# Kernel tuning notes

Measured on AMD Instinct MI355X. Metric: run time of the kernel, lower is better.

## Reference

```python
import jax, jax.numpy as jnp
import numpy as np
import math

D_MODEL = 1024
N_HEADS = 16
HEAD_DIM = D_MODEL // N_HEADS
SEQ = 2048
BATCH = 4
MAX_SEQ_LEN = 2048
THETA = 10000.0


def setup_inputs() -> dict:
    key = jax.random.key(0)
    ks = jax.random.split(key, 5)
    std = math.sqrt(2.0 / (D_MODEL + D_MODEL))
    x = jax.random.normal(ks[0], (BATCH, SEQ, D_MODEL), dtype=jnp.float32)
    wq = jax.random.normal(ks[1], (D_MODEL, D_MODEL), dtype=jnp.float32) * std
    wk = jax.random.normal(ks[2], (D_MODEL, D_MODEL), dtype=jnp.float32) * std
    wv = jax.random.normal(ks[3], (D_MODEL, D_MODEL), dtype=jnp.float32) * std
    wo = jax.random.normal(ks[4], (D_MODEL, D_MODEL), dtype=jnp.float32) * std
    token_positions = jnp.arange(SEQ, dtype=jnp.int32)
    return {"x": x, "token_positions": token_positions,
            "wq": wq, "wk": wk, "wv": wv, "wo": wo}


def _rope_tables(token_positions):
    # thetas_i = 1 / theta^(2i/d_k), angles[p, i] = p * thetas_i
    thetas = 1.0 / (THETA ** (2.0 * jnp.arange(HEAD_DIM // 2, dtype=jnp.float32) / HEAD_DIM))
    positions = jnp.arange(MAX_SEQ_LEN, dtype=jnp.float32)
    angles = jnp.outer(positions, thetas)  # [max_seq, d_k/2]
    cos = jnp.cos(angles)[token_positions]  # [S, d_k/2]
    sin = jnp.sin(angles)[token_positions]
    return cos, sin


def _apply_rope(x, cos, sin):
    # x: [B, H, S, D]; pairs (even, odd) form complex numbers
    shp = x.shape
    x2 = x.reshape(*shp[:-1], HEAD_DIM // 2, 2)
    xe, xo = x2[..., 0], x2[..., 1]
    re = xe * cos - xo * sin
    im = xe * sin + xo * cos
    return jnp.stack([re, im], axis=-1).reshape(shp)


def reference(x, token_positions, wq, wk, wv, wo):
    B, S, _ = x.shape
    # LinearNoBias: einsum('...j,ij->...i', x, W)
    q = jnp.einsum('bsj,ij->bsi', x, wq)
    k = jnp.einsum('bsj,ij->bsi', x, wk)
    v = jnp.einsum('bsj,ij->bsi', x, wv)
    # split heads -> [B, H, S, D]
    q = q.reshape(B, S, N_HEADS, HEAD_DIM).transpose(0, 2, 1, 3)
    k = k.reshape(B, S, N_HEADS, HEAD_DIM).transpose(0, 2, 1, 3)
    v = v.reshape(B, S, N_HEADS, HEAD_DIM).transpose(0, 2, 1, 3)
    cos, sin = _rope_tables(token_positions)
    q = _apply_rope(q, cos, sin)
    k = _apply_rope(k, cos, sin)
    scores = jnp.einsum('bhqd,bhkd->bhqk', q, k) / math.sqrt(HEAD_DIM)
    causal = jnp.tril(jnp.ones((S, S), dtype=bool))
    scores = jnp.where(causal, scores, -jnp.inf)
    probs = jax.nn.softmax(scores, axis=-1)
    out = jnp.einsum('bhqk,bhkd->bhqd', probs, v)
    out = out.transpose(0, 2, 1, 3).reshape(B, S, N_HEADS * HEAD_DIM)
    return jnp.einsum('bsj,ij->bsi', out, wo)
```

## Files before the change

### kernel.cpp

```cpp
#include <hip/hip_runtime.h>
#include <stdint.h>

#define B_SZ 4
#define S_LEN 2048
#define NH 16
#define HD 64
#define DM 1024

typedef __bf16 bf16;
typedef __bf16 bf16x4 __attribute__((ext_vector_type(4)));
typedef __bf16 bf16x8 __attribute__((ext_vector_type(8)));
typedef float f32x4 __attribute__((ext_vector_type(4)));

#define MFMA16(a, b, c) __builtin_amdgcn_mfma_f32_16x16x32_bf16(a, b, c, 0, 0, 0)

__device__ __forceinline__ void gl2lds16(const void* g, void* l) {
  __builtin_amdgcn_global_load_lds(
      (__attribute__((address_space(1))) const void*)g,
      (__attribute__((address_space(3))) void*)l, 16, 0, 0);
}

__device__ __forceinline__ void bar_lgkm() {
  asm volatile("s_waitcnt lgkmcnt(0)\n\ts_barrier" ::: "memory");
}

__device__ __forceinline__ bf16x8 ldcvt(const float* p) {
  f32x4 u0 = *(const f32x4*)p;
  f32x4 u1 = *(const f32x4*)(p + 4);
  bf16x8 v;
#pragma unroll
  for (int j = 0; j < 4; j++) {
    v[j] = (bf16)u0[j];
    v[4 + j] = (bf16)u1[j];
  }
  return v;
}

__global__ void cvt_kernel(const float* __restrict__ x,
                           const float* __restrict__ wq,
                           const float* __restrict__ wk,
                           const float* __restrict__ wv,
                           const float* __restrict__ wo,
                           bf16* __restrict__ Xb, bf16* __restrict__ Wb,
                           long xN) {
  const long e = ((long)blockIdx.x * 256 + threadIdx.x) * 8;
  const float* src;
  bf16* dst;
  long off;
  if (e < xN) {
    src = x; dst = Xb; off = e;
  } else {
    const long w = e - xN;
    const int wi = (int)(w >> 20);
    src = (wi == 0) ? wq : (wi == 1) ? wk : (wi == 2) ? wv : wo;
    dst = Wb + ((size_t)wi << 20);
    off = w & ((1L << 20) - 1);
  }
  *(bf16x8*)(dst + off) = ldcvt(src + off);
}

__device__ __forceinline__ void gemm_core_bb(const bf16* __restrict__ Ag,
                                             const bf16* __restrict__ Bg,
                                             f32x4 acc[4][4], bf16* As,
                                             bf16* Bs) {
  const int tid = threadIdx.x;
  const int lane = tid & 63;
  const int wave = tid >> 6;
  const int wm = (wave >> 1) * 64;
  const int wn = (wave & 1) * 64;
  const int col = lane & 15;
  const int kq = (lane >> 4) * 8;
  const int r0 = tid >> 2;
  const int c0 = (tid & 3) * 8;
#pragma unroll
  for (int i = 0; i < 4; i++)
#pragma unroll
    for (int j = 0; j < 4; j++) acc[i][j] = (f32x4){0.f, 0.f, 0.f, 0.f};

  gl2lds16(Ag + (size_t)r0 * 1024 + c0, As + tid * 8);
  gl2lds16(Ag + (size_t)(r0 + 64) * 1024 + c0, As + 2048 + tid * 8);
  gl2lds16(Bg + (size_t)r0 * 1024 + c0, Bs + tid * 8);
  gl2lds16(Bg + (size_t)(r0 + 64) * 1024 + c0, Bs + 2048 + tid * 8);

  for (int ki = 0; ki < 32; ki++) {
    bar_lgkm();
    if (ki + 1 < 32) {
      const int kn = (ki + 1) * 32;
      bf16* Ad = As + ((ki + 1) & 1) * 4096;
      bf16* Bd = Bs + ((ki + 1) & 1) * 4096;
      gl2lds16(Ag + (size_t)r0 * 1024 + kn + c0, Ad + tid * 8);
      gl2lds16(Ag + (size_t)(r0 + 64) * 1024 + kn + c0, Ad + 2048 + tid * 8);
      gl2lds16(Bg + (size_t)r0 * 1024 + kn + c0, Bd + tid * 8);
      gl2lds16(Bg + (size_t)(r0 + 64) * 1024 + kn + c0, Bd + 2048 + tid * 8);
      asm volatile("s_waitcnt vmcnt(4)" ::: "memory");
    } else {
      asm volatile("s_waitcnt vmcnt(0)" ::: "memory");
    }
    asm volatile("s_barrier" ::: "memory");

    const bf16* Ac = As + (ki & 1) * 4096;
    const bf16* Bc = Bs + (ki & 1) * 4096;
    bf16x8 af[4], bfr[4];
#pragma unroll
    for (int i = 0; i < 4; i++)
      af[i] = *(const bf16x8*)(Ac + (wm + i * 16 + col) * 32 + kq);
#pragma unroll
    for (int j = 0; j < 4; j++)
      bfr[j] = *(const bf16x8*)(Bc + (wn + j * 16 + col) * 32 + kq);
#pragma unroll
    for (int i = 0; i < 4; i++)
#pragma unroll
      for (int j = 0; j < 4; j++)
        acc[i][j] = MFMA16(af[i], bfr[j], acc[i][j]);
  }
}

__global__ __launch_bounds__(256, 4) void qkv_gemm(
    const bf16* __restrict__ x, const bf16* __restrict__ Wb,
    const int* __restrict__ tp, bf16* __restrict__ Q, bf16* __restrict__ K,
    bf16* __restrict__ Vt) {
  __shared__ __align__(16) bf16 As[2 * 128 * 32];
  __shared__ __align__(16) bf16 Bs[2 * 128 * 32];
  const int bx = blockIdx.x;
  const int by = blockIdx.y;
  const int wsel = by >> 3;
  const int n0 = (by & 7) * 128;

  f32x4 acc[4][4];
  gemm_core_bb(x + (size_t)bx * 128 * 1024,
               Wb + ((size_t)wsel << 20) + (size_t)n0 * 1024, acc, As, Bs);

  const int lane = threadIdx.x & 63;
  const int wave = threadIdx.x >> 6;
  const int wm = (wave >> 1) * 64, wn = (wave & 1) * 64;
  const int col = lane & 15, quad = lane >> 4;

  if (wsel < 2) {
    bf16* dst = wsel ? K : Q;
    const float qs = wsel ? 1.0f : 0.18033688011112042f;
    const int codd = col & 1;
    float freqs[4];
#pragma unroll
    for (int j = 0; j < 4; j++)
      freqs[j] = __builtin_exp2f(-(float)(j * 8 + (col >> 1)) *
                                 0.41524101186091903f);
#pragma unroll
    for (int i = 0; i < 4; i++) {
      const int m0 = bx * 128 + wm + i * 16 + quad * 4;
#pragma unroll
      for (int r = 0; r < 4; r++) {
        const int mm = m0 + r;
        const int bl = mm >> 11, s = mm & 2047;
        const float pf = (float)tp[s];
#pragma unroll
        for (int j = 0; j < 4; j++) {
          const int n = n0 + wn + j * 16 + col;
          const int h = n >> 6, d = n & 63;
          const float own = acc[i][j][r];
          const float oth = __shfl_xor(own, 1);
          const float ang = pf * freqs[j];
          const float mine = codd ? __cosf(ang) : __sinf(ang);
          const float thr = __shfl_xor(mine, 1);
          const float sn = codd ? thr : mine;
          const float cn = codd ? mine : thr;
          const float res = codd ? (oth * sn + own * cn) : (own * cn - oth * sn);
          dst[((((size_t)bl * NH + h) * S_LEN + s) << 6) + d] =
              (bf16)(res * qs);
        }
      }
    }
  } else {
#pragma unroll
    for (int i = 0; i < 4; i++) {
      const int m0 = bx * 128 + wm + i * 16 + quad * 4;
      const int bl = m0 >> 11, s = m0 & 2047;
#pragma unroll
      for (int j = 0; j < 4; j++) {
        const int n = n0 + wn + j * 16 + col;
        const int h = n >> 6, d = n & 63;
        bf16x4 pk;
#pragma unroll
        for (int r = 0; r < 4; r++) pk[r] = (bf16)acc[i][j][r];
        *(bf16x4*)(Vt + (((size_t)(bl * NH + h) * 64 + d) << 11) + s) = pk;
      }
    }
  }
}

#define PP 72
__global__ __launch_bounds__(256, 2) void attn_kernel(
    const bf16* __restrict__ Q, const bf16* __restrict__ K,
    const bf16* __restrict__ Vt, bf16* __restrict__ O) {
  __shared__ __align__(16) bf16 Kb[2][64 * 64];
  __shared__ __align__(16) bf16 Vb[2][64 * 64];
  __shared__ __align__(16) bf16 Ps[4 * 32 * PP];

  const int tid = threadIdx.x, lane = tid & 63, wave = tid >> 6;
  const int col = lane & 15, quad = lane >> 4, kq = quad * 8;
  const int bh = blockIdx.x;
  const int yb = blockIdx.y;
  const int qt = (yb < 8) ? (15 - yb) : (yb - 8);
  const int bl = bh >> 4, h = bh & 15;
  const bf16* Kg = K + (size_t)bh * S_LEN * 64;
  const bf16* Vg = Vt + (size_t)bh * 64 * S_LEN;
  bf16* Pw = Ps + wave * 32 * PP;
  const int wq_abs = qt * 128 + wave * 32;
  const int qmax = wq_abs + 31;

  const int r_ = tid >> 3;
  const int cs_ = (tid & 7) ^ (r_ & 7);
  const int kx = col & 7;

  const bf16* Qg = Q + ((size_t)bh * S_LEN + wq_abs) * 64;
  bf16x8 qf[2][2];
#pragma unroll
  for (int mi = 0; mi < 2; mi++)
#pragma unroll
    for (int kc = 0; kc < 2; kc++)
      qf[mi][kc] =
          *(const bf16x8*)(Qg + (mi * 16 + col) * 64 + kc * 32 + kq);

  f32x4 oacc[2][4];
  float lst[2] = {0.f, 0.f};
#pragma unroll
  for (int mi = 0; mi < 2; mi++)
#pragma unroll
    for (int nd = 0; nd < 4; nd++) oacc[mi][nd] = (f32x4){0.f, 0.f, 0.f, 0.f};

  const int ntiles = 2 * qt + 2;

  gl2lds16(Kg + (size_t)r_ * 64 + cs_ * 8, Kb[0] + tid * 8);
  gl2lds16(Kg + (size_t)(r_ + 32) * 64 + cs_ * 8, Kb[0] + 2048 + tid * 8);
  gl2lds16(Vg + (size_t)r_ * S_LEN + cs_ * 8, Vb[0] + tid * 8);
  gl2lds16(Vg + (size_t)(r_ + 32) * S_LEN + cs_ * 8, Vb[0] + 2048 + tid * 8);

  for (int kt = 0; kt < ntiles; kt++) {
    bar_lgkm();
    if (kt + 1 < ntiles) {
      bf16* kd = Kb[(kt + 1) & 1];
      bf16* vd = Vb[(kt + 1) & 1];
      const bf16* Kn = Kg + (size_t)(kt + 1) * 64 * 64;
      const bf16* Vn = Vg + (kt + 1) * 64;
      gl2lds16(Kn + (size_t)r_ * 64 + cs_ * 8, kd + tid * 8);
      gl2lds16(Kn + (size_t)(r_ + 32) * 64 + cs_ * 8, kd + 2048 + tid * 8);
      gl2lds16(Vn + (size_t)r_ * S_LEN + cs_ * 8, vd + tid * 8);
      gl2lds16(Vn + (size_t)(r_ + 32) * S_LEN + cs_ * 8, vd + 2048 + tid * 8);
      asm volatile("s_waitcnt vmcnt(4)" ::: "memory");
    } else {
      asm volatile("s_waitcnt vmcnt(0)" ::: "memory");
    }
    asm volatile("s_barrier" ::: "memory");

    const int kb = kt * 64;
    if (kb > qmax) continue;
    const bf16* Kc = Kb[kt & 1];
    const bf16* Vc = Vb[kt & 1];

    f32x4 sa[2][4];
#pragma unroll
    for (int ni = 0; ni < 4; ni++) {
      const int krow = ni * 16 + col;
      bf16x8 kf0 = *(const bf16x8*)(Kc + krow * 64 + ((quad ^ kx) << 3));
      bf16x8 kf1 =
          *(const bf16x8*)(Kc + krow * 64 + (((quad + 4) ^ kx) << 3));
#pragma unroll
      for (int mi = 0; mi < 2; mi++) {
        f32x4 s = {0.f, 0.f, 0.f, 0.f};
        s = MFMA16(kf0, qf[mi][0], s);
        s = MFMA16(kf1, qf[mi][1], s);
        sa[mi][ni] = s;
      }
    }
    if (kb + 63 > wq_abs) {
      const int base = kb - wq_abs + quad * 4;
#pragma unroll
      for (int mi = 0; mi < 2; mi++)
#pragma unroll
        for (int ni = 0; ni < 4; ni++)
#pragma unroll
          for (int r = 0; r < 4; r++)
            if (base + ni * 16 + r > mi * 16 + col) sa[mi][ni][r] = -1e30f;
    }
#pragma unroll
    for (int mi = 0; mi < 2; mi++) {
      float rs = 0.f;
#pragma unroll
      for (int ni = 0; ni < 4; ni++)
#pragma unroll
        for (int r = 0; r < 4; r++) {
          float pv = __builtin_exp2f(sa[mi][ni][r]);
          sa[mi][ni][r] = pv;
          rs += pv;
        }
      lst[mi] += rs;
    }
#pragma unroll
    for (int mi = 0; mi < 2; mi++)
#pragma unroll
      for (int ni = 0; ni < 4; ni++) {
        bf16x4 pk;
#pragma unroll
        for (int r = 0; r < 4; r++) pk[r] = (bf16)sa[mi][ni][r];
        *(bf16x4*)(Pw + (mi * 16 + col) * PP + ni * 16 + quad * 4) = pk;
      }
#pragma unroll
    for (int kcl = 0; kcl < 2; kcl++) {
      bf16x8 pf[2];
#pragma unroll
      for (int mi = 0; mi < 2; mi++)
        pf[mi] = *(const bf16x8*)(Pw + (mi * 16 + col) * PP + kcl * 32 + kq);
#pragma unroll
      for (int nd = 0; nd < 4; nd++) {
        const int vrow = nd * 16 + col;
        bf16x8 vf = *(const bf16x8*)(Vc + vrow * 64 +
                                     (((kcl * 4 + quad) ^ kx) << 3));
#pragma unroll
        for (int mi = 0; mi < 2; mi++)
          oacc[mi][nd] = MFMA16(pf[mi], vf, oacc[mi][nd]);
      }
    }
  }

#pragma unroll
  for (int mi = 0; mi < 2; mi++) {
    float rs = lst[mi];
    rs += __shfl_xor(rs, 16);
    rs += __shfl_xor(rs, 32);
    const float il = 1.0f / rs;
    float linv[4];
#pragma unroll
    for (int r = 0; r < 4; r++) linv[r] = __shfl(il, quad * 4 + r);
    const int srow0 = wq_abs + mi * 16 + quad * 4;
#pragma unroll
    for (int nd = 0; nd < 4; nd++)
#pragma unroll
      for (int r = 0; r < 4; r++)
        O[(size_t)(bl * S_LEN + srow0 + r) * DM + h * 64 + nd * 16 + col] =
            (bf16)(oacc[mi][nd][r] * linv[r]);
  }
}

__global__ __launch_bounds__(256, 4) void out_gemm(const bf16* __restrict__ A,
                                                   const bf16* __restrict__ W,
                                                   float* __restrict__ out) {
  __shared__ __align__(16) bf16 As[2 * 128 * 32];
  __shared__ __align__(16) bf16 Bs[2 * 128 * 32];
  f32x4 acc[4][4];
  gemm_core_bb(A + (size_t)blockIdx.x * 128 * 1024,
               W + (size_t)blockIdx.y * 128 * 1024, acc, As, Bs);
  const int lane = threadIdx.x & 63;
  const int wave = threadIdx.x >> 6;
  const int wm = (wave >> 1) * 64, wn = (wave & 1) * 64;
  const int col = lane & 15, quad = lane >> 4;
#pragma unroll
  for (int i = 0; i < 4; i++) {
    const int m0 = blockIdx.x * 128 + wm + i * 16 + quad * 4;
#pragma unroll
    for (int j = 0; j < 4; j++) {
      const int n = blockIdx.y * 128 + wn + j * 16 + col;
#pragma unroll
      for (int r = 0; r < 4; r++)
        out[(size_t)(m0 + r) * DM + n] = acc[i][j][r];
    }
  }
}

extern "C" void kernel_launch(void* const* d_in, const int* in_sizes, int n_in,
                              void* d_out, int out_size, void* d_ws,
                              size_t ws_size, hipStream_t stream) {
  const float* x = (const float*)d_in[0];
  const int* tp = (const int*)d_in[1];
  const float* wq = (const float*)d_in[2];
  const float* wk = (const float*)d_in[3];
  const float* wv = (const float*)d_in[4];
  const float* wo = (const float*)d_in[5];
  float* out = (float*)d_out;
  bf16* wsb = (bf16*)d_ws;

  const size_t TENb = (size_t)NH * S_LEN * HD;
  const size_t WSZ = 4ull * DM * DM;
  int bcnt = 1;
  if (ws_size >= (4 * 4 * TENb + WSZ) * sizeof(bf16)) bcnt = 4;
  else if (ws_size >= (4 * 2 * TENb + WSZ) * sizeof(bf16)) bcnt = 2;

  const size_t REG = (size_t)bcnt * TENb;
  bf16* Xb = wsb;
  bf16* Qw = wsb + REG;
  bf16* Kw = wsb + 2 * REG;
  bf16* Vtw = wsb + 3 * REG;
  bf16* Wb = wsb + 4 * REG;
  bf16* Ow = Xb;

  for (int b0 = 0; b0 < B_SZ; b0 += bcnt) {
    const float* xb = x + (size_t)b0 * S_LEN * DM;
    float* outb = out + (size_t)b0 * S_LEN * DM;
    const long cvtN = (long)(REG + WSZ);
    hipLaunchKernelGGL(cvt_kernel, dim3((unsigned)(cvtN / 2048)), dim3(256), 0,
                       stream, xb, wq, wk, wv, wo, Xb, Wb, (long)REG);
    hipLaunchKernelGGL(qkv_gemm, dim3(bcnt * 16, 24), dim3(256), 0, stream,
                       Xb, Wb, tp, Qw, Kw, Vtw);
    hipLaunchKernelGGL(attn_kernel, dim3(bcnt * 16, 16), dim3(256), 0, stream,
                       Qw, Kw, Vtw, Ow);
    hipLaunchKernelGGL(out_gemm, dim3(bcnt * 16, 8), dim3(256), 0, stream,
                       Ow, Wb + 3ull * DM * DM, outb);
  }
}
```

Measured before the change: 255.1 us.

## Enlarge QKV GEMM tiles to 256x256 with 512 threads and swizzled LDS

```diff
diff --git a/kernel.cpp b/kernel.cpp
--- a/kernel.cpp
+++ b/kernel.cpp
@@ -115,26 +115,80 @@
   }
 }
 
-__global__ __launch_bounds__(256, 4) void qkv_gemm(
+__global__ __launch_bounds__(512, 2) void qkv_gemm(
     const bf16* __restrict__ x, const bf16* __restrict__ Wb,
     const int* __restrict__ tp, bf16* __restrict__ Q, bf16* __restrict__ K,
     bf16* __restrict__ Vt) {
-  __shared__ __align__(16) bf16 As[2 * 128 * 32];
-  __shared__ __align__(16) bf16 Bs[2 * 128 * 32];
+  __shared__ __align__(16) bf16 As[2][256 * 64];
+  __shared__ __align__(16) bf16 Bs[2][256 * 64];
+
+  const int tid = threadIdx.x;
+  const int lane = tid & 63;
+  const int wid = tid >> 6;
+  const int wr = wid >> 2;
+  const int wc = wid & 3;
+  const int col = lane & 15, quad = lane >> 4;
   const int bx = blockIdx.x;
   const int by = blockIdx.y;
-  const int wsel = by >> 3;
-  const int n0 = (by & 7) * 128;
-
-  f32x4 acc[4][4];
-  gemm_core_bb(x + (size_t)bx * 128 * 1024,
-               Wb + ((size_t)wsel << 20) + (size_t)n0 * 1024, acc, As, Bs);
-
-  const int lane = threadIdx.x & 63;
-  const int wave = threadIdx.x >> 6;
-  const int wm = (wave >> 1) * 64, wn = (wave & 1) * 64;
-  const int col = lane & 15, quad = lane >> 4;
-
+  const int wsel = by >> 2;
+  const int n0 = (by & 3) * 256;
+  const bf16* Ag = x + (size_t)bx * 256 * 1024;
+  const bf16* Bg = Wb + ((size_t)wsel << 20) + (size_t)n0 * 1024;
+
+  const int sr = tid >> 3;
+  const int sc = (tid & 7) ^ (sr & 7);
+
+  f32x4 acc[8][4];
+#pragma unroll
+  for (int i = 0; i < 8; i++)
+#pragma unroll
+    for (int j = 0; j < 4; j++) acc[i][j] = (f32x4){0.f, 0.f, 0.f, 0.f};
+
+  auto stage = [&](int b, int kt) {
+    const int k0 = kt * 64;
+#pragma unroll
+    for (int ch = 0; ch < 4; ch++) {
+      gl2lds16(Ag + (size_t)(ch * 64 + sr) * 1024 + k0 + sc * 8,
+               &As[b][ch * 4096 + tid * 8]);
+      gl2lds16(Bg + (size_t)(ch * 64 + sr) * 1024 + k0 + sc * 8,
+               &Bs[b][ch * 4096 + tid * 8]);
+    }
+  };
+
+  stage(0, 0);
+  for (int kt = 0; kt < 16; kt++) {
+    bar_lgkm();
+    if (kt + 1 < 16) {
+      stage((kt + 1) & 1, kt + 1);
+      asm volatile("s_waitcnt vmcnt(8)" ::: "memory");
+    } else {
+      asm volatile("s_waitcnt vmcnt(0)" ::: "memory");
+    }
+    asm volatile("s_barrier" ::: "memory");
+
+    const bf16* Ac = As[kt & 1];
+    const bf16* Bc = Bs[kt & 1];
+#pragma unroll
+    for (int ks = 0; ks < 2; ks++) {
+      bf16x8 bfr[4];
+#pragma unroll
+      for (int j = 0; j < 4; j++) {
+        const int row = wc * 64 + j * 16 + col;
+        bfr[j] = *(const bf16x8*)(Bc + row * 64 +
+                                  (((ks * 4 + quad) ^ (col & 7)) << 3));
+      }
+#pragma unroll
+      for (int i = 0; i < 8; i++) {
+        const int row = wr * 128 + i * 16 + col;
+        bf16x8 af = *(const bf16x8*)(Ac + row * 64 +
+                                     (((ks * 4 + quad) ^ (col & 7)) << 3));
+#pragma unroll
+        for (int j = 0; j < 4; j++) acc[i][j] = MFMA16(af, bfr[j], acc[i][j]);
+      }
+    }
+  }
+
+  const int h = (by & 3) * 4 + wc;
   if (wsel < 2) {
     bf16* dst = wsel ? K : Q;
     const float qs = wsel ? 1.0f : 0.18033688011112042f;
@@ -145,8 +199,8 @@
       freqs[j] = __builtin_exp2f(-(float)(j * 8 + (col >> 1)) *
                                  0.41524101186091903f);
 #pragma unroll
-    for (int i = 0; i < 4; i++) {
-      const int m0 = bx * 128 + wm + i * 16 + quad * 4;
+    for (int i = 0; i < 8; i++) {
+      const int m0 = bx * 256 + wr * 128 + i * 16 + quad * 4;
 #pragma unroll
       for (int r = 0; r < 4; r++) {
         const int mm = m0 + r;
@@ -154,8 +208,7 @@
         const float pf = (float)tp[s];
 #pragma unroll
         for (int j = 0; j < 4; j++) {
-          const int n = n0 + wn + j * 16 + col;
-          const int h = n >> 6, d = n & 63;
+          const int d = j * 16 + col;
           const float own = acc[i][j][r];
           const float oth = __shfl_xor(own, 1);
           const float ang = pf * freqs[j];
@@ -163,7 +216,8 @@
           const float thr = __shfl_xor(mine, 1);
           const float sn = codd ? thr : mine;
           const float cn = codd ? mine : thr;
-          const float res = codd ? (oth * sn + own * cn) : (own * cn - oth * sn);
+          const float res =
+              codd ? (oth * sn + own * cn) : (own * cn - oth * sn);
           dst[((((size_t)bl * NH + h) * S_LEN + s) << 6) + d] =
               (bf16)(res * qs);
         }
@@ -171,13 +225,12 @@
     }
   } else {
 #pragma unroll
-    for (int i = 0; i < 4; i++) {
-      const int m0 = bx * 128 + wm + i * 16 + quad * 4;
+    for (int i = 0; i < 8; i++) {
+      const int m0 = bx * 256 + wr * 128 + i * 16 + quad * 4;
       const int bl = m0 >> 11, s = m0 & 2047;
 #pragma unroll
       for (int j = 0; j < 4; j++) {
-        const int n = n0 + wn + j * 16 + col;
-        const int h = n >> 6, d = n & 63;
+        const int d = j * 16 + col;
         bf16x4 pk;
 #pragma unroll
         for (int r = 0; r < 4; r++) pk[r] = (bf16)acc[i][j][r];
@@ -397,7 +450,7 @@
     const long cvtN = (long)(REG + WSZ);
     hipLaunchKernelGGL(cvt_kernel, dim3((unsigned)(cvtN / 2048)), dim3(256), 0,
                        stream, xb, wq, wk, wv, wo, Xb, Wb, (long)REG);
-    hipLaunchKernelGGL(qkv_gemm, dim3(bcnt * 16, 24), dim3(256), 0, stream,
+    hipLaunchKernelGGL(qkv_gemm, dim3(bcnt * 8, 12), dim3(512), 0, stream,
                        Xb, Wb, tp, Qw, Kw, Vtw);
     hipLaunchKernelGGL(attn_kernel, dim3(bcnt * 16, 16), dim3(256), 0, stream,
                        Qw, Kw, Vtw, Ow);
```

Result: slower. 265.2 us (+4.0%).
